# Kernel optimization log

Hardware: AMD Instinct MI355X
Metric: run time of the kernel (lower is better)

## Reference

```python
import jax, jax.numpy as jnp
import numpy as np
from math import factorial, sqrt

# ---- configuration (matches init_kwargs) ----
MUL = 64
N = 32768
IRREPS1 = [(MUL, l) for l in range(3)]   # 64x0e + 64x1o + 64x2e
IRREPS2 = [(1, l) for l in range(3)]     # 1x0e + 1x1o + 1x2e (spherical harmonics)
IRREPS_OUT = [(MUL, l) for l in range(3)]
# (i_in1, i_in2, i_out) -- all parity/triangle-allowed uvw paths with l<=2
PATHS = [(0,0,0),(0,1,1),(0,2,2),(1,0,1),(1,1,0),(1,1,2),(1,2,1),(2,0,2),(2,1,1),(2,2,0),(2,2,2)]

# ---- real Clebsch-Gordan (e3nn convention: real basis, unit Frobenius norm) ----
def _su2_cg(j1, m1, j2, m2, j3, m3):
    if m3 != m1 + m2:
        return 0.0
    f = factorial
    vmin = max(-j1 + j2 + m3, -j1 + m1, 0)
    vmax = min(j2 + j3 + m1, j3 - j1 + j2, j3 + m3)
    C = sqrt((2*j3+1) * f(j3+j1-j2) * f(j3-j1+j2) * f(j1+j2-j3) * f(j3+m3) * f(j3-m3)
             / (f(j1+j2+j3+1) * f(j1-m1) * f(j1+m1) * f(j2-m2) * f(j2+m2)))
    S = 0.0
    for v in range(vmin, vmax + 1):
        S += (-1.0)**(v + j2 + m2) * f(j2+j3+m1-v) * f(j1-m1+v) / (f(v) * f(j3-j1+j2-v) * f(j3+m3-v) * f(v+j1-j2-m3))
    return C * S

def _su2_clebsch_gordan(j1, j2, j3):
    mat = np.zeros((2*j1+1, 2*j2+1, 2*j3+1))
    for m1 in range(-j1, j1+1):
        for m2 in range(-j2, j2+1):
            if abs(m1 + m2) <= j3:
                mat[j1+m1, j2+m2, j3+m1+m2] = _su2_cg(j1, m1, j2, m2, j3, m1+m2)
    return mat

def _change_basis_real_to_complex(l):
    q = np.zeros((2*l+1, 2*l+1), dtype=np.complex128)
    for m in range(-l, 0):
        q[l+m, l+abs(m)] = 1/sqrt(2)
        q[l+m, l-abs(m)] = -1j/sqrt(2)
    q[l, l] = 1
    for m in range(1, l+1):
        q[l+m, l+abs(m)] = (-1)**m / sqrt(2)
        q[l+m, l-abs(m)] = 1j * (-1)**m / sqrt(2)
    return (-1j)**l * q

def clebsch_gordan(l1, l2, l3):
    Q1 = _change_basis_real_to_complex(l1)
    Q2 = _change_basis_real_to_complex(l2)
    Q3 = _change_basis_real_to_complex(l3)
    C = _su2_clebsch_gordan(l1, l2, l3)
    C = np.einsum('ij,kl,mn,ikn->jlm', Q1, Q2, np.conj(Q3.T), C)
    C = np.real(C)
    return C / np.linalg.norm(C)  # unit Frobenius norm (e3nn convention)

# ---- static layout / path weights ----
def _offsets(irreps):
    offs, s = [], 0
    for mul, l in irreps:
        offs.append(s)
        s += mul * (2*l + 1)
    return offs

OFF1, OFF2, OFFO = _offsets(IRREPS1), _offsets(IRREPS2), _offsets(IRREPS_OUT)
# path_normalization='element', irrep_normalization='component'
_norm = {}
for (i1, i2, io) in PATHS:
    _norm[io] = _norm.get(io, 0) + IRREPS1[i1][0] * IRREPS2[i2][0]
PW = [sqrt((2*IRREPS_OUT[io][1] + 1) / _norm[io]) for (_, _, io) in PATHS]


def setup_inputs() -> dict:
    key = jax.random.key(0)
    k1, k2, k3 = jax.random.split(key, 3)
    dim1 = sum(m * (2*l+1) for m, l in IRREPS1)  # 576
    dim2 = sum(m * (2*l+1) for m, l in IRREPS2)  # 9
    nw = sum(IRREPS1[i1][0] * IRREPS2[i2][0] * IRREPS_OUT[io][0] for (i1, i2, io) in PATHS)
    x1 = jax.random.normal(k1, (N, dim1), dtype=jnp.float32)
    x2 = jax.random.normal(k2, (N, dim2), dtype=jnp.float32)
    weights = jax.random.normal(k3, (nw,), dtype=jnp.float32)
    return {"x1": x1, "x2": x2, "weights": weights}


def reference(x1, x2, weights):
    out_acc = [None] * len(IRREPS_OUT)
    wi = 0
    for (i1, i2, io), pw in zip(PATHS, PW):
        m1, l1 = IRREPS1[i1]
        m2, l2 = IRREPS2[i2]
        mo, lo = IRREPS_OUT[io]
        npar = m1 * m2 * mo
        w = weights[wi:wi + npar].reshape(m1, m2, mo)
        wi += npar
        # per-irrep chunks: [N, mul, 2l+1]
        x1c = x1[:, OFF1[i1]:OFF1[i1] + m1 * (2*l1+1)].reshape(-1, m1, 2*l1+1)
        x2c = x2[:, OFF2[i2]:OFF2[i2] + m2 * (2*l2+1)].reshape(-1, m2, 2*l2+1)
        cg = jnp.asarray(pw * clebsch_gordan(l1, l2, lo), dtype=x1.dtype)
        out = jnp.einsum('uvw,ijk,nui,nvj->nwk', w, cg, x1c, x2c)
        out_acc[io] = out if out_acc[io] is None else out_acc[io] + out
    return jnp.concatenate([o.reshape(o.shape[0], -1) for o in out_acc], axis=1)
```

## Files before the change

kernel.cpp:

```cpp
#include <hip/hip_runtime.h>
#include <hip/hip_bf16.h>

#define NDIM1 576
#define NDIM2 9
#define NDIMO 576

typedef __attribute__((ext_vector_type(8))) short short8;
typedef __attribute__((ext_vector_type(4))) float f32x4;

union U8 { unsigned short s[8]; short8 v; };

__device__ inline unsigned short f2bf(float x) {
  return __builtin_bit_cast(unsigned short, __float2bfloat16(x));
}

constexpr bool cg_nonzero(int m1, int m2, int m3) {
  int a1 = m1 < 0 ? -m1 : m1, a2 = m2 < 0 ? -m2 : m2, a3 = m3 < 0 ? -m3 : m3;
  int d = a1 > a2 ? a1 - a2 : a2 - a1;
  bool mag = (a3 == a1 + a2) || (a3 == d);
  int neg = (m1 < 0) + (m2 < 0) + (m3 < 0);
  return mag && ((neg & 1) == 0);
}

constexpr double cfact(int n) { double r = 1.0; for (int i = 2; i <= n; i++) r *= (double)i; return r; }
constexpr double csqrt_(double x) {
  if (x <= 0.0) return 0.0;
  double g = x < 1.0 ? 1.0 : x;
  for (int i = 0; i < 60; i++) g = 0.5 * (g + x / g);
  return g;
}
constexpr int cmax3(int a, int b, int c) { int m = a > b ? a : b; return m > c ? m : c; }
constexpr int cmin3(int a, int b, int c) { int m = a < b ? a : b; return m < c ? m : c; }

struct cpx { double re; double im; };
constexpr cpx operator*(cpx a, cpx b) { return {a.re * b.re - a.im * b.im, a.re * b.im + a.im * b.re}; }
constexpr cpx operator+(cpx a, cpx b) { return {a.re + b.re, a.im + b.im}; }
constexpr cpx cconj(cpx a) { return {a.re, -a.im}; }
constexpr cpx cscale(cpx a, double s) { return {a.re * s, a.im * s}; }

constexpr double su2_cg_c(int j1, int m1, int j2, int m2, int j3, int m3) {
  if (m3 != m1 + m2) return 0.0;
  int vmin = cmax3(-j1 + j2 + m3, -j1 + m1, 0);
  int vmax = cmin3(j2 + j3 + m1, j3 - j1 + j2, j3 + m3);
  double C = csqrt_((2.0 * j3 + 1.0) * cfact(j3 + j1 - j2) * cfact(j3 - j1 + j2) *
                    cfact(j1 + j2 - j3) * cfact(j3 + m3) * cfact(j3 - m3) /
                    (cfact(j1 + j2 + j3 + 1) * cfact(j1 - m1) * cfact(j1 + m1) *
                     cfact(j2 - m2) * cfact(j2 + m2)));
  double S = 0.0;
  for (int vv = vmin; vv <= vmax; vv++) {
    double sg = ((vv + j2 + m2) & 1) ? -1.0 : 1.0;
    S += sg * cfact(j2 + j3 + m1 - vv) * cfact(j1 - m1 + vv) /
         (cfact(vv) * cfact(j3 - j1 + j2 - vv) * cfact(j3 + m3 - vv) * cfact(vv + j1 - j2 - m3));
  }
  return C * S;
}

struct QM { cpx q[5][5]; };
constexpr QM cb_r2c_c(int l) {
  QM m{};
  const double is2 = 1.0 / csqrt_(2.0);
  for (int mm = -l; mm < 0; mm++) {
    m.q[l + mm][l - mm] = {is2, 0.0};
    m.q[l + mm][l + mm] = {0.0, -is2};
  }
  m.q[l][l] = {1.0, 0.0};
  for (int mm = 1; mm <= l; mm++) {
    double sg = (mm & 1) ? -1.0 : 1.0;
    m.q[l + mm][l + mm] = {sg * is2, 0.0};
    m.q[l + mm][l - mm] = {0.0, sg * is2};
  }
  cpx f{1.0, 0.0};
  for (int t = 0; t < l; t++) f = f * cpx{0.0, -1.0};
  for (int a = 0; a < 2 * l + 1; a++)
    for (int b = 0; b < 2 * l + 1; b++) m.q[a][b] = m.q[a][b] * f;
  return m;
}

struct C555 { double v[5][5][5]; };
constexpr C555 cg_real_c(int l1, int l2, int l3) {
  QM q1 = cb_r2c_c(l1), q2 = cb_r2c_c(l2), q3 = cb_r2c_c(l3);
  double su[5][5][5]{};
  for (int i = 0; i < 2 * l1 + 1; i++)
    for (int k = 0; k < 2 * l2 + 1; k++)
      for (int n = 0; n < 2 * l3 + 1; n++)
        su[i][k][n] = su2_cg_c(l1, i - l1, l2, k - l2, l3, n - l3);
  C555 o{};
  double nrm = 0.0;
  for (int x = 0; x < 2 * l1 + 1; x++)
    for (int y = 0; y < 2 * l2 + 1; y++)
      for (int z = 0; z < 2 * l3 + 1; z++) {
        cpx a{0.0, 0.0};
        for (int i = 0; i < 2 * l1 + 1; i++)
          for (int k = 0; k < 2 * l2 + 1; k++)
            for (int n = 0; n < 2 * l3 + 1; n++) {
              double s = su[i][k][n];
              if (s != 0.0) a = a + cscale(q1.q[i][x] * q2.q[k][y] * cconj(q3.q[n][z]), s);
            }
        o.v[x][y][z] = a.re;
        nrm += a.re * a.re;
      }
  nrm = csqrt_(nrm);
  for (int x = 0; x < 2 * l1 + 1; x++)
    for (int y = 0; y < 2 * l2 + 1; y++)
      for (int z = 0; z < 2 * l3 + 1; z++) o.v[x][y][z] /= nrm;
  return o;
}

static constexpr C555 CGP0 = cg_real_c(0, 0, 0);
static constexpr C555 CGP1 = cg_real_c(0, 1, 1);
static constexpr C555 CGP2 = cg_real_c(0, 2, 2);
static constexpr C555 CGP3 = cg_real_c(1, 0, 1);
static constexpr C555 CGP4 = cg_real_c(1, 1, 0);
static constexpr C555 CGP5 = cg_real_c(1, 1, 2);
static constexpr C555 CGP6 = cg_real_c(1, 2, 1);
static constexpr C555 CGP7 = cg_real_c(2, 0, 2);
static constexpr C555 CGP8 = cg_real_c(2, 1, 1);
static constexpr C555 CGP9 = cg_real_c(2, 2, 0);
static constexpr C555 CGP10 = cg_real_c(2, 2, 2);

struct CGTabC { float v[363]; };
constexpr CGTabC build_flat() {
  CGTabC t{};
  const C555* cp[11] = {&CGP0, &CGP1, &CGP2, &CGP3, &CGP4, &CGP5, &CGP6, &CGP7, &CGP8, &CGP9, &CGP10};
  const int PL1[11] = {0, 0, 0, 1, 1, 1, 1, 2, 2, 2, 2};
  const int PL2[11] = {0, 1, 2, 0, 1, 1, 2, 0, 1, 2, 2};
  const int PLO[11] = {0, 1, 2, 1, 0, 2, 1, 2, 1, 0, 2};
  const int CGO[11] = {0, 1, 10, 35, 44, 53, 98, 143, 168, 213, 238};
  const double pw_io[3] = {csqrt_(1.0 / 192.0), csqrt_(3.0 / 256.0), csqrt_(5.0 / 256.0)};
  for (int p = 0; p < 11; p++) {
    int l1 = PL1[p], l2 = PL2[p], lo = PLO[p];
    double pw = pw_io[lo];
    for (int i = 0; i < 2 * l1 + 1; i++)
      for (int j = 0; j < 2 * l2 + 1; j++)
        for (int k = 0; k < 2 * lo + 1; k++)
          t.v[CGO[p] + (i * (2 * l2 + 1) + j) * (2 * lo + 1) + k] = (float)(pw * cp[p]->v[i][j][k]);
  }
  return t;
}
static constexpr CGTabC CGT = build_flat();

__global__ __launch_bounds__(256) void prep_w_kernel(const float* __restrict__ W,
                                                     short8* __restrict__ wf) {
  int idx = blockIdx.x * 256 + threadIdx.x;
  if (idx >= 11 * 2 * 4 * 64) return;
  int lane = idx & 63;
  int v = (idx >> 6) & 3;
  int s = (idx >> 8) & 1;
  int p = idx >> 9;
  int g = lane >> 4, r16 = lane & 15;
  const float* wp = W + p * 4096 + (s * 32 + g * 8) * 64 + v * 16 + r16;
  U8 u;
#pragma unroll
  for (int t = 0; t < 8; t++) u.s[t] = f2bf(wp[t * 64]);
  wf[idx] = u.v;
}

__device__ __forceinline__ void stage_issue(const float* __restrict__ x1, int nt,
                                            int wv, int g, int r16, f32x4 (&raw)[12]) {
  const float* row = x1 + (size_t)(nt * 16 + r16) * NDIM1;
  if (wv == 0) {
#pragma unroll
    for (int s = 0; s < 2; s++) {
      const f32x4* p = (const f32x4*)(row + (s * 32 + g * 8));
      raw[s * 2 + 0] = p[0];
      raw[s * 2 + 1] = p[1];
    }
  } else if (wv == 1) {
#pragma unroll
    for (int s = 0; s < 2; s++) {
      const f32x4* p = (const f32x4*)(row + 64 + (s * 32 + g * 8) * 3);
#pragma unroll
      for (int q = 0; q < 6; q++) raw[s * 6 + q] = p[q];
    }
  } else {
    const int s = wv - 2;
    const f32x4* p = (const f32x4*)(row + 256 + (s * 32 + g * 8) * 5);
#pragma unroll
    for (int q = 0; q < 10; q++) raw[q] = p[q];
  }
}

__device__ __forceinline__ void stage_write(short8 (*fb)[64], int wv, int lane,
                                            const f32x4 (&raw)[12]) {
  const float* rf = (const float*)raw;
  if (wv == 0) {
#pragma unroll
    for (int s = 0; s < 2; s++) {
      U8 u;
#pragma unroll
      for (int t = 0; t < 8; t++) u.s[t] = f2bf(rf[s * 8 + t]);
      fb[s][lane] = u.v;
    }
  } else if (wv == 1) {
#pragma unroll
    for (int s = 0; s < 2; s++)
#pragma unroll
      for (int i = 0; i < 3; i++) {
        U8 u;
#pragma unroll
        for (int t = 0; t < 8; t++) u.s[t] = f2bf(rf[s * 24 + t * 3 + i]);
        fb[2 + s * 3 + i][lane] = u.v;
      }
  } else {
    const int s = wv - 2;
#pragma unroll
    for (int i = 0; i < 5; i++) {
      U8 u;
#pragma unroll
      for (int t = 0; t < 8; t++) u.s[t] = f2bf(rf[t * 5 + i]);
      fb[8 + s * 5 + i][lane] = u.v;
    }
  }
}

template <int NI>
__device__ __forceinline__ void run_path(const short8* __restrict__ wf, int p, int v, int lane,
                                         const short8 (&af)[NI][2], f32x4 (&acc)[NI]) {
#pragma unroll
  for (int i = 0; i < NI; i++) acc[i] = (f32x4){0.f, 0.f, 0.f, 0.f};
#pragma unroll
  for (int s = 0; s < 2; s++) {
    short8 b = wf[((p * 2 + s) * 4 + v) * 64 + lane];
#pragma unroll
    for (int i = 0; i < NI; i++)
      acc[i] = __builtin_amdgcn_mfma_f32_16x16x32_bf16(af[i][s], b, acc[i], 0, 0, 0);
  }
}

template <int L1, int L2, int LO, int CGO, int NI>
__device__ __forceinline__ void epilogue(const f32x4 (&acc)[NI],
                                         const float (&x2v)[4][9], float (&outr)[4][9]) {
  constexpr int JO = (L2 == 0) ? 0 : (L2 == 1 ? 1 : 4);
  constexpr int KO = (LO == 0) ? 0 : (LO == 1 ? 1 : 4);
#pragma unroll
  for (int i = 0; i < 2 * L1 + 1; i++) {
#pragma unroll
    for (int j = 0; j < 2 * L2 + 1; j++) {
#pragma unroll
      for (int k = 0; k < 2 * LO + 1; k++) {
        if (!cg_nonzero(i - L1, j - L2, k - LO)) continue;
        float c = CGT.v[CGO + (i * (2 * L2 + 1) + j) * (2 * LO + 1) + k];
#pragma unroll
        for (int r = 0; r < 4; r++)
          outr[r][KO + k] = fmaf(c * x2v[r][JO + j], acc[i][r], outr[r][KO + k]);
      }
    }
  }
}

__device__ __forceinline__ void compute_tile(const short8 (*fb)[64],
                                             const float* __restrict__ x2,
                                             const short8* __restrict__ wf,
                                             float* __restrict__ out,
                                             int n0, int v, int lane, int g, int r16) {
  f32x4 xv[9];
  {
    const f32x4* p2 = (const f32x4*)(x2 + (size_t)(n0 + g * 4) * NDIM2);
#pragma unroll
    for (int q = 0; q < 9; q++) xv[q] = p2[q];
  }
  float x2v[4][9];
  float outr[4][9];
#pragma unroll
  for (int r = 0; r < 4; r++)
#pragma unroll
    for (int j = 0; j < 9; j++) {
      int idx = r * 9 + j;
      x2v[r][j] = xv[idx >> 2][idx & 3];
      outr[r][j] = 0.f;
    }

  {
    short8 af[1][2]; f32x4 acc[1];
#pragma unroll
    for (int s = 0; s < 2; s++) af[0][s] = fb[s][lane];
    run_path<1>(wf, 0, v, lane, af, acc); epilogue<0, 0, 0, 0, 1>(acc, x2v, outr);
    run_path<1>(wf, 1, v, lane, af, acc); epilogue<0, 1, 1, 1, 1>(acc, x2v, outr);
    run_path<1>(wf, 2, v, lane, af, acc); epilogue<0, 2, 2, 10, 1>(acc, x2v, outr);
  }
  {
    short8 af[3][2]; f32x4 acc[3];
#pragma unroll
    for (int s = 0; s < 2; s++)
#pragma unroll
      for (int i = 0; i < 3; i++) af[i][s] = fb[2 + s * 3 + i][lane];
    run_path<3>(wf, 3, v, lane, af, acc); epilogue<1, 0, 1, 35, 3>(acc, x2v, outr);
    run_path<3>(wf, 4, v, lane, af, acc); epilogue<1, 1, 0, 44, 3>(acc, x2v, outr);
    run_path<3>(wf, 5, v, lane, af, acc); epilogue<1, 1, 2, 53, 3>(acc, x2v, outr);
    run_path<3>(wf, 6, v, lane, af, acc); epilogue<1, 2, 1, 98, 3>(acc, x2v, outr);
  }
  {
    short8 af[5][2]; f32x4 acc[5];
#pragma unroll
    for (int s = 0; s < 2; s++)
#pragma unroll
      for (int i = 0; i < 5; i++) af[i][s] = fb[8 + s * 5 + i][lane];
    run_path<5>(wf, 7, v, lane, af, acc); epilogue<2, 0, 2, 143, 5>(acc, x2v, outr);
    run_path<5>(wf, 8, v, lane, af, acc); epilogue<2, 1, 1, 168, 5>(acc, x2v, outr);
    run_path<5>(wf, 9, v, lane, af, acc); epilogue<2, 2, 0, 213, 5>(acc, x2v, outr);
    run_path<5>(wf, 10, v, lane, af, acc); epilogue<2, 2, 2, 238, 5>(acc, x2v, outr);
  }

  const int w = v * 16 + r16;
#pragma unroll
  for (int r = 0; r < 4; r++) {
    float* op = out + (size_t)(n0 + g * 4 + r) * NDIMO;
    op[w] = outr[r][0];
#pragma unroll
    for (int k = 0; k < 3; k++) op[64 + w * 3 + k] = outr[r][1 + k];
#pragma unroll
    for (int k = 0; k < 5; k++) op[256 + w * 5 + k] = outr[r][4 + k];
  }
}

__global__ __launch_bounds__(256) void TPWithWeights_44925357916441_kernel(
    const float* __restrict__ x1, const float* __restrict__ x2,
    const short8* __restrict__ wf, float* __restrict__ out) {
  __shared__ short8 frg[2][18][64];

  const int lane = threadIdx.x & 63;
  const int wv = threadIdx.x >> 6;
  const int g = lane >> 4, r16 = lane & 15;
  const int t0 = blockIdx.x * 2;

  {
    f32x4 rawA[12];
    stage_issue(x1, t0, wv, g, r16, rawA);
    stage_write(frg[0], wv, lane, rawA);
  }
  __syncthreads();

  {
    f32x4 rawB[12];
    stage_issue(x1, t0 + 1, wv, g, r16, rawB);
    compute_tile(frg[0], x2, wf, out, t0 << 4, wv, lane, g, r16);
    stage_write(frg[1], wv, lane, rawB);
  }
  __syncthreads();

  compute_tile(frg[1], x2, wf, out, (t0 + 1) << 4, wv, lane, g, r16);
}

extern "C" void kernel_launch(void* const* d_in, const int* in_sizes, int n_in,
                              void* d_out, int out_size, void* d_ws, size_t ws_size,
                              hipStream_t stream) {
  const float* x1 = (const float*)d_in[0];
  const float* x2 = (const float*)d_in[1];
  const float* W  = (const float*)d_in[2];
  float* out = (float*)d_out;

  int N = in_sizes[0] / NDIM1;

  short8* wf = (short8*)d_ws;

  hipLaunchKernelGGL(prep_w_kernel, dim3(22), dim3(256), 0, stream, W, wf);
  hipLaunchKernelGGL(TPWithWeights_44925357916441_kernel, dim3(N / 32), dim3(256), 0,
                     stream, x1, x2, wf, out);
}
```

Measured before the change: 48.95 us.

## Use 2-wave blocks of one 16-row tile, dropping the two-tile software pipeline

Each block now has two wavefronts and handles a single 16-row tile instead of four wavefronts handling two tiles with overlapped staging. Each wave stages twice the x1 data (l0+l1 or two l2 halves) and runs compute_tile for two output-column groups in sequence. The grid doubles and shared memory per block halves, giving more, smaller blocks for the scheduler. The cost is losing the overlap of the next tile's loads with compute, plus larger per-thread register staging (20 vectors instead of 12).

```diff
diff --git a/kernel.cpp b/kernel.cpp
--- a/kernel.cpp
+++ b/kernel.cpp
@@ -155,8 +155,8 @@
   wf[idx] = u.v;
 }
 
-__device__ __forceinline__ void stage_issue(const float* __restrict__ x1, int nt,
-                                            int wv, int g, int r16, f32x4 (&raw)[12]) {
+__device__ __forceinline__ void stage_issue2(const float* __restrict__ x1, int nt,
+                                             int wv, int g, int r16, f32x4 (&raw)[20]) {
   const float* row = x1 + (size_t)(nt * 16 + r16) * NDIM1;
   if (wv == 0) {
 #pragma unroll
@@ -165,23 +165,24 @@
       raw[s * 2 + 0] = p[0];
       raw[s * 2 + 1] = p[1];
     }
-  } else if (wv == 1) {
 #pragma unroll
     for (int s = 0; s < 2; s++) {
       const f32x4* p = (const f32x4*)(row + 64 + (s * 32 + g * 8) * 3);
 #pragma unroll
-      for (int q = 0; q < 6; q++) raw[s * 6 + q] = p[q];
+      for (int q = 0; q < 6; q++) raw[4 + s * 6 + q] = p[q];
     }
   } else {
-    const int s = wv - 2;
-    const f32x4* p = (const f32x4*)(row + 256 + (s * 32 + g * 8) * 5);
-#pragma unroll
-    for (int q = 0; q < 10; q++) raw[q] = p[q];
-  }
-}
-
-__device__ __forceinline__ void stage_write(short8 (*fb)[64], int wv, int lane,
-                                            const f32x4 (&raw)[12]) {
+#pragma unroll
+    for (int s = 0; s < 2; s++) {
+      const f32x4* p = (const f32x4*)(row + 256 + (s * 32 + g * 8) * 5);
+#pragma unroll
+      for (int q = 0; q < 10; q++) raw[s * 10 + q] = p[q];
+    }
+  }
+}
+
+__device__ __forceinline__ void stage_write2(short8 (*fb)[64], int wv, int lane,
+                                             const f32x4 (&raw)[20]) {
   const float* rf = (const float*)raw;
   if (wv == 0) {
 #pragma unroll
@@ -191,25 +192,25 @@
       for (int t = 0; t < 8; t++) u.s[t] = f2bf(rf[s * 8 + t]);
       fb[s][lane] = u.v;
     }
-  } else if (wv == 1) {
 #pragma unroll
     for (int s = 0; s < 2; s++)
 #pragma unroll
       for (int i = 0; i < 3; i++) {
         U8 u;
 #pragma unroll
-        for (int t = 0; t < 8; t++) u.s[t] = f2bf(rf[s * 24 + t * 3 + i]);
+        for (int t = 0; t < 8; t++) u.s[t] = f2bf(rf[16 + s * 24 + t * 3 + i]);
         fb[2 + s * 3 + i][lane] = u.v;
       }
   } else {
-    const int s = wv - 2;
-#pragma unroll
-    for (int i = 0; i < 5; i++) {
-      U8 u;
-#pragma unroll
-      for (int t = 0; t < 8; t++) u.s[t] = f2bf(rf[t * 5 + i]);
-      fb[8 + s * 5 + i][lane] = u.v;
-    }
+#pragma unroll
+    for (int s = 0; s < 2; s++)
+#pragma unroll
+      for (int i = 0; i < 5; i++) {
+        U8 u;
+#pragma unroll
+        for (int t = 0; t < 8; t++) u.s[t] = f2bf(rf[s * 40 + t * 5 + i]);
+        fb[8 + s * 5 + i][lane] = u.v;
+      }
   }
 }
 
@@ -313,32 +314,25 @@
   }
 }
 
-__global__ __launch_bounds__(256) void TPWithWeights_44925357916441_kernel(
+__global__ __launch_bounds__(128) void TPWithWeights_44925357916441_kernel(
     const float* __restrict__ x1, const float* __restrict__ x2,
     const short8* __restrict__ wf, float* __restrict__ out) {
-  __shared__ short8 frg[2][18][64];
+  __shared__ short8 frg[18][64];
 
   const int lane = threadIdx.x & 63;
   const int wv = threadIdx.x >> 6;
   const int g = lane >> 4, r16 = lane & 15;
-  const int t0 = blockIdx.x * 2;
-
-  {
-    f32x4 rawA[12];
-    stage_issue(x1, t0, wv, g, r16, rawA);
-    stage_write(frg[0], wv, lane, rawA);
+  const int n0 = blockIdx.x << 4;
+
+  {
+    f32x4 raw[20];
+    stage_issue2(x1, blockIdx.x, wv, g, r16, raw);
+    stage_write2(frg, wv, lane, raw);
   }
   __syncthreads();
 
-  {
-    f32x4 rawB[12];
-    stage_issue(x1, t0 + 1, wv, g, r16, rawB);
-    compute_tile(frg[0], x2, wf, out, t0 << 4, wv, lane, g, r16);
-    stage_write(frg[1], wv, lane, rawB);
-  }
-  __syncthreads();
-
-  compute_tile(frg[1], x2, wf, out, (t0 + 1) << 4, wv, lane, g, r16);
+  compute_tile(frg, x2, wf, out, n0, wv * 2 + 0, lane, g, r16);
+  compute_tile(frg, x2, wf, out, n0, wv * 2 + 1, lane, g, r16);
 }
 
 extern "C" void kernel_launch(void* const* d_in, const int* in_sizes, int n_in,
@@ -354,6 +348,6 @@
   short8* wf = (short8*)d_ws;
 
   hipLaunchKernelGGL(prep_w_kernel, dim3(22), dim3(256), 0, stream, W, wf);
-  hipLaunchKernelGGL(TPWithWeights_44925357916441_kernel, dim3(N / 32), dim3(256), 0,
+  hipLaunchKernelGGL(TPWithWeights_44925357916441_kernel, dim3(N / 16), dim3(128), 0,
                      stream, x1, x2, wf, out);
 }
```

After: 52.63 us. 1.08x slower.

## Stage output tile through LDS for coalesced stores, one tile per block

Applied to the files above, without the earlier changes.

Each block now handles one 16-row tile instead of two, which drops the software-pipelined prefetch of the second tile and doubles the grid size. Results are written to a shared-memory buffer (reusing the fragment area) and then copied to global memory with contiguous 16-byte vector stores, replacing strided scalar stores. The aim is to improve write coalescing, since output is the largest stream. The cost is extra barriers and LDS traffic, plus the loss of load/compute overlap within a block.

```diff
diff --git a/kernel.cpp b/kernel.cpp
--- a/kernel.cpp
+++ b/kernel.cpp
@@ -248,11 +248,11 @@
   }
 }
 
-__device__ __forceinline__ void compute_tile(const short8 (*fb)[64],
-                                             const float* __restrict__ x2,
-                                             const short8* __restrict__ wf,
-                                             float* __restrict__ out,
-                                             int n0, int v, int lane, int g, int r16) {
+__device__ __forceinline__ void compute_tile_regs(const short8 (*fb)[64],
+                                                  const float* __restrict__ x2,
+                                                  const short8* __restrict__ wf,
+                                                  int n0, int v, int lane, int g,
+                                                  float (&outr)[4][9]) {
   f32x4 xv[9];
   {
     const f32x4* p2 = (const f32x4*)(x2 + (size_t)(n0 + g * 4) * NDIM2);
@@ -260,7 +260,6 @@
     for (int q = 0; q < 9; q++) xv[q] = p2[q];
   }
   float x2v[4][9];
-  float outr[4][9];
 #pragma unroll
   for (int r = 0; r < 4; r++)
 #pragma unroll
@@ -300,45 +299,52 @@
     run_path<5>(wf, 9, v, lane, af, acc); epilogue<2, 2, 0, 213, 5>(acc, x2v, outr);
     run_path<5>(wf, 10, v, lane, af, acc); epilogue<2, 2, 2, 238, 5>(acc, x2v, outr);
   }
-
-  const int w = v * 16 + r16;
-#pragma unroll
-  for (int r = 0; r < 4; r++) {
-    float* op = out + (size_t)(n0 + g * 4 + r) * NDIMO;
-    op[w] = outr[r][0];
-#pragma unroll
-    for (int k = 0; k < 3; k++) op[64 + w * 3 + k] = outr[r][1 + k];
-#pragma unroll
-    for (int k = 0; k < 5; k++) op[256 + w * 5 + k] = outr[r][4 + k];
-  }
 }
 
 __global__ __launch_bounds__(256) void TPWithWeights_44925357916441_kernel(
     const float* __restrict__ x1, const float* __restrict__ x2,
     const short8* __restrict__ wf, float* __restrict__ out) {
-  __shared__ short8 frg[2][18][64];
+  __shared__ __align__(16) char smem[36864];
+  short8 (*frg)[64] = (short8(*)[64])smem;
+  float* outs = (float*)smem;
 
   const int lane = threadIdx.x & 63;
   const int wv = threadIdx.x >> 6;
   const int g = lane >> 4, r16 = lane & 15;
-  const int t0 = blockIdx.x * 2;
-
-  {
-    f32x4 rawA[12];
-    stage_issue(x1, t0, wv, g, r16, rawA);
-    stage_write(frg[0], wv, lane, rawA);
+  const int n0 = blockIdx.x << 4;
+
+  {
+    f32x4 raw[12];
+    stage_issue(x1, blockIdx.x, wv, g, r16, raw);
+    stage_write(frg, wv, lane, raw);
   }
   __syncthreads();
 
-  {
-    f32x4 rawB[12];
-    stage_issue(x1, t0 + 1, wv, g, r16, rawB);
-    compute_tile(frg[0], x2, wf, out, t0 << 4, wv, lane, g, r16);
-    stage_write(frg[1], wv, lane, rawB);
-  }
+  float outr[4][9];
+  compute_tile_regs(frg, x2, wf, n0, wv, lane, g, outr);
   __syncthreads();
 
-  compute_tile(frg[1], x2, wf, out, (t0 + 1) << 4, wv, lane, g, r16);
+  {
+    const int w = wv * 16 + r16;
+#pragma unroll
+    for (int r = 0; r < 4; r++) {
+      float* op = outs + (g * 4 + r) * NDIMO;
+      op[w] = outr[r][0];
+#pragma unroll
+      for (int k = 0; k < 3; k++) op[64 + w * 3 + k] = outr[r][1 + k];
+#pragma unroll
+      for (int k = 0; k < 5; k++) op[256 + w * 5 + k] = outr[r][4 + k];
+    }
+  }
+  __syncthreads();
+
+  {
+    f32x4* gb4 = (f32x4*)(out + (size_t)n0 * NDIMO);
+    const f32x4* lb4 = (const f32x4*)outs;
+    const int tid = threadIdx.x;
+#pragma unroll
+    for (int it = 0; it < 9; it++) gb4[it * 256 + tid] = lb4[it * 256 + tid];
+  }
 }
 
 extern "C" void kernel_launch(void* const* d_in, const int* in_sizes, int n_in,
@@ -354,6 +360,6 @@
   short8* wf = (short8*)d_ws;
 
   hipLaunchKernelGGL(prep_w_kernel, dim3(22), dim3(256), 0, stream, W, wf);
-  hipLaunchKernelGGL(TPWithWeights_44925357916441_kernel, dim3(N / 32), dim3(256), 0,
+  hipLaunchKernelGGL(TPWithWeights_44925357916441_kernel, dim3(N / 16), dim3(256), 0,
                      stream, x1, x2, wf, out);
 }
```

Measured after the change: 61.17 us. 25.0% more time.
